# Optimization experiments

Hardware: AMD Instinct MI355X
Metric: run time of the kernel (lower is better)

Reference implementation:

```python
import jax, jax.numpy as jnp
import numpy as np

N, DIN, DOUT = 8192, 256, 128
NEG_SLOPE = 0.01         # F.leaky_relu default
MASK_VAL = -9.0e15       # from the torch source


def setup_inputs() -> dict:
    key = jax.random.key(0)
    kx, kadj, kW, kbW, ka1, ka2, kba = jax.random.split(key, 7)
    x = jax.random.normal(kx, (N, DIN), dtype=jnp.float32)
    adj = jax.random.randint(kadj, (N, N), 0, 2, dtype=jnp.int32)
    # Linear W: input_dim -> output_dim
    W = jax.random.normal(kW, (DIN, DOUT), dtype=jnp.float32) * (1.0 / np.sqrt(DIN))
    bW = jax.random.normal(kbW, (DOUT,), dtype=jnp.float32) * 0.01
    # Linear a: 2*output_dim -> 1, split into the h_i part (a1) and h_j part (a2)
    a1 = jax.random.normal(ka1, (DOUT,), dtype=jnp.float32) * (1.0 / np.sqrt(2 * DOUT))
    a2 = jax.random.normal(ka2, (DOUT,), dtype=jnp.float32) * (1.0 / np.sqrt(2 * DOUT))
    ba = jax.random.normal(kba, (), dtype=jnp.float32) * 0.01
    return {"x": x, "adj": adj, "W": W, "bW": bW, "a1": a1, "a2": a2, "ba": ba}


def reference(x, adj, W, bW, a1, a2, ba):
    # h = W x + b  -> [N, DOUT]
    h = x @ W + bW
    # e[i,j] = leaky_relu(a . [h_i, h_j] + ba) = leaky_relu(a1.h_i + a2.h_j + ba)
    s_src = h @ a1            # [N]
    s_dst = h @ a2            # [N]
    e = s_src[:, None] + s_dst[None, :] + ba   # [N, N]
    e = jnp.where(e > 0, e, NEG_SLOPE * e)
    # mask non-edges, row softmax over neighbors j
    e = jnp.where(adj > 0, e, MASK_VAL)
    alpha = jax.nn.softmax(e, axis=1)          # [N, N]
    # dropout is identity in eval mode (dropout_rate=0)
    return alpha @ h                            # [N, DOUT]
```

## Files before the change

kernel.cpp:

```cpp
#include <hip/hip_runtime.h>
#include <hip/hip_bf16.h>


#define NN 8192
#define DIN 256
#define DOUT 128

typedef __attribute__((ext_vector_type(8))) short short8;
typedef __attribute__((ext_vector_type(4))) float floatx4;

__global__ void prep_wt(const float* __restrict__ W, __hip_bfloat16* __restrict__ WT) {
    int e = blockIdx.x * blockDim.x + threadIdx.x;
    if (e < DIN * DOUT) {
        int k = e >> 7;
        int d = e & 127;
        WT[d * DIN + k] = __float2bfloat16(W[e]);
    }
}

__global__ __launch_bounds__(256, 4) void gat_h(
    const float* __restrict__ x, const __hip_bfloat16* __restrict__ WT,
    const float* __restrict__ bW, const float* __restrict__ a1, const float* __restrict__ a2,
    __hip_bfloat16* __restrict__ hbT, float* __restrict__ s_src, float* __restrict__ s_dst) {
    int tid = threadIdx.x;
    int w = tid >> 6, lane = tid & 63;
    int lm = lane & 15, lq = lane >> 4;
    int i0 = blockIdx.x * 32;
    int r0 = (w >> 1) * 16;
    int c0 = (w & 1) * 64;

    __shared__ float s1s[32], s2s[32];
    if (tid < 32) { s1s[tid] = 0.f; s2s[tid] = 0.f; }
    __syncthreads();

    floatx4 acc[4] = {};
#pragma unroll
    for (int kk = 0; kk < DIN; kk += 32) {
        const float4* xp = (const float4*)&x[(size_t)(i0 + r0 + lm) * DIN + kk + lq * 8];
        float4 xa = xp[0], xb = xp[1];
        union { short8 v; __hip_bfloat16 h[8]; } af;
        af.h[0] = __float2bfloat16(xa.x); af.h[1] = __float2bfloat16(xa.y);
        af.h[2] = __float2bfloat16(xa.z); af.h[3] = __float2bfloat16(xa.w);
        af.h[4] = __float2bfloat16(xb.x); af.h[5] = __float2bfloat16(xb.y);
        af.h[6] = __float2bfloat16(xb.z); af.h[7] = __float2bfloat16(xb.w);
#pragma unroll
        for (int t = 0; t < 4; t++) {
            int d = c0 + 16 * t + lm;
            short8 bf = *(const short8*)&WT[(size_t)d * DIN + kk + lq * 8];
            acc[t] = __builtin_amdgcn_mfma_f32_16x16x32_bf16(af.v, bf, acc[t], 0, 0, 0);
        }
    }
    float s1[4] = {0.f, 0.f, 0.f, 0.f}, s2[4] = {0.f, 0.f, 0.f, 0.f};
#pragma unroll
    for (int t = 0; t < 4; t++) {
        int d = c0 + 16 * t + lm;
        float A1 = a1[d], A2 = a2[d], B = bW[d];
#pragma unroll
        for (int r = 0; r < 4; r++) {
            int row = r0 + lq * 4 + r;
            float h = acc[t][r] + B;
            hbT[(size_t)d * NN + i0 + row] = __float2bfloat16(h);
            s1[r] += h * A1;
            s2[r] += h * A2;
        }
    }
#pragma unroll
    for (int r = 0; r < 4; r++) {
        for (int m = 1; m < 16; m <<= 1) {
            s1[r] += __shfl_xor(s1[r], m, 64);
            s2[r] += __shfl_xor(s2[r], m, 64);
        }
    }
    if (lm == 0) {
#pragma unroll
        for (int r = 0; r < 4; r++) {
            int row = r0 + lq * 4 + r;
            atomicAdd(&s1s[row], s1[r]);
            atomicAdd(&s2s[row], s2[r]);
        }
    }
    __syncthreads();
    if (tid < 32) {
        s_src[i0 + tid] = s1s[tid];
        s_dst[i0 + tid] = s2s[tid];
    }
}

__global__ __launch_bounds__(256, 4) void gat_attn(
    const int* __restrict__ adj, const float* __restrict__ s_src,
    const float* __restrict__ s_dst, const float* __restrict__ ba_p,
    const __hip_bfloat16* __restrict__ hbT,
    float* __restrict__ num, float* __restrict__ lpart, int njt) {
    int tid = threadIdx.x;
    int w = tid >> 6, lane = tid & 63;
    int lm = lane & 15, lq = lane >> 4;
    int b = blockIdx.x;
    int ib = b & 127;
    int jh = b >> 7;
    int i0 = ib * 64 + w * 16;
    int jb0 = jh * (njt * 32);

    float ssi = s_src[i0 + lm] + ba_p[0];

    const int* arow = adj + (size_t)(i0 + lm) * NN + jb0 + lq * 8;
    const float* sd = s_dst + jb0 + lq * 8;
    const __hip_bfloat16* hbb = hbT + (size_t)lm * NN + jb0 + lq * 8;

    floatx4 acc[8] = {};
    floatx4 accd = {};
    const short8 ones = { 0x3F80, 0x3F80, 0x3F80, 0x3F80, 0x3F80, 0x3F80, 0x3F80, 0x3F80 };

    int4 a0 = *(const int4*)arow;
    int4 a1 = *(const int4*)(arow + 4);
    float4 d0 = *(const float4*)sd;
    float4 d1 = *(const float4*)(sd + 4);

    for (int t = 0; t < njt; t++) {
        int4 ca0 = a0, ca1 = a1;
        float4 cd0 = d0, cd1 = d1;
        if (t + 1 < njt) {
            a0 = *(const int4*)(arow + (t + 1) * 32);
            a1 = *(const int4*)(arow + (t + 1) * 32 + 4);
            d0 = *(const float4*)(sd + (t + 1) * 32);
            d1 = *(const float4*)(sd + (t + 1) * 32 + 4);
        }
        float p[8];
        {
            float e;
            e = ssi + cd0.x; e = fmaxf(e, 0.01f * e); p[0] = ca0.x ? __expf(e) : 0.f;
            e = ssi + cd0.y; e = fmaxf(e, 0.01f * e); p[1] = ca0.y ? __expf(e) : 0.f;
            e = ssi + cd0.z; e = fmaxf(e, 0.01f * e); p[2] = ca0.z ? __expf(e) : 0.f;
            e = ssi + cd0.w; e = fmaxf(e, 0.01f * e); p[3] = ca0.w ? __expf(e) : 0.f;
            e = ssi + cd1.x; e = fmaxf(e, 0.01f * e); p[4] = ca1.x ? __expf(e) : 0.f;
            e = ssi + cd1.y; e = fmaxf(e, 0.01f * e); p[5] = ca1.y ? __expf(e) : 0.f;
            e = ssi + cd1.z; e = fmaxf(e, 0.01f * e); p[6] = ca1.z ? __expf(e) : 0.f;
            e = ssi + cd1.w; e = fmaxf(e, 0.01f * e); p[7] = ca1.w ? __expf(e) : 0.f;
        }
        union { short8 v; __hip_bfloat162 q[4]; } af;
        af.q[0] = __float22bfloat162_rn(make_float2(p[0], p[1]));
        af.q[1] = __float22bfloat162_rn(make_float2(p[2], p[3]));
        af.q[2] = __float22bfloat162_rn(make_float2(p[4], p[5]));
        af.q[3] = __float22bfloat162_rn(make_float2(p[6], p[7]));

        size_t off = (size_t)t * 32;
#pragma unroll
        for (int f = 0; f < 8; f++) {
            short8 bf = *(const short8*)(hbb + (size_t)f * 16 * NN + off);
            acc[f] = __builtin_amdgcn_mfma_f32_16x16x32_bf16(af.v, bf, acc[f], 0, 0, 0);
        }
        accd = __builtin_amdgcn_mfma_f32_16x16x32_bf16(af.v, ones, accd, 0, 0, 0);
    }

    float* nb = num + ((size_t)jh * NN + i0) * DOUT;
#pragma unroll
    for (int f = 0; f < 8; f++)
#pragma unroll
        for (int r = 0; r < 4; r++)
            nb[(size_t)(lq * 4 + r) * DOUT + f * 16 + lm] = acc[f][r];
    if (lm == 0) {
#pragma unroll
        for (int r = 0; r < 4; r++)
            lpart[(size_t)jh * NN + i0 + lq * 4 + r] = accd[r];
    }
}

__global__ void gat_combine(const float* __restrict__ num, const float* __restrict__ lpart,
                            float* __restrict__ out, int jsplit) {
    int gid = blockIdx.x * blockDim.x + threadIdx.x;
    int idx = gid * 4;
    int i = idx >> 7;
    float den = 0.f;
    for (int s = 0; s < jsplit; s++) den += lpart[(size_t)s * NN + i];
    float inv = 1.0f / den;
    float4 o = make_float4(0.f, 0.f, 0.f, 0.f);
    for (int s = 0; s < jsplit; s++) {
        float4 n = *(const float4*)&num[(size_t)s * NN * DOUT + idx];
        o.x += n.x; o.y += n.y; o.z += n.z; o.w += n.w;
    }
    o.x *= inv; o.y *= inv; o.z *= inv; o.w *= inv;
    *(float4*)&out[idx] = o;
}

extern "C" void kernel_launch(void* const* d_in, const int* in_sizes, int n_in,
                              void* d_out, int out_size, void* d_ws, size_t ws_size,
                              hipStream_t stream) {
    const float* x  = (const float*)d_in[0];
    const int* adj  = (const int*)d_in[1];
    const float* W  = (const float*)d_in[2];
    const float* bW = (const float*)d_in[3];
    const float* a1 = (const float*)d_in[4];
    const float* a2 = (const float*)d_in[5];
    const float* ba = (const float*)d_in[6];
    float* out = (float*)d_out;

    char* ws = (char*)d_ws;
    __hip_bfloat16* hbT = (__hip_bfloat16*)ws;
    __hip_bfloat16* WT  = (__hip_bfloat16*)(ws + 2097152);
    float* s_src        = (float*)(ws + 2162688);
    float* s_dst        = (float*)(ws + 2195456);
    float* lpart        = (float*)(ws + 2228224);
    float* num          = (float*)(ws + 2490368);

    size_t base = 2490368;
    int jsplit = 2;
    if (ws_size >= base + (size_t)8 * NN * DOUT * 4) jsplit = 8;
    else if (ws_size >= base + (size_t)4 * NN * DOUT * 4) jsplit = 4;
    int njt = NN / (32 * jsplit);

    prep_wt<<<128, 256, 0, stream>>>(W, WT);
    gat_h<<<256, 256, 0, stream>>>(x, WT, bW, a1, a2, hbT, s_src, s_dst);
    gat_attn<<<128 * jsplit, 256, 0, stream>>>(adj, s_src, s_dst, ba, hbT, num, lpart, njt);
    gat_combine<<<1024, 256, 0, stream>>>(num, lpart, out, jsplit);
}
```

Baseline: 512.3 us.

## Pack adjacency into a bitmask in a prepass and template the attention kernel on tile count

Adds a streaming build_mask kernel that compresses each run of eight int32 adjacency entries into a single byte bitmask. The attention kernel then reads one byte per eight columns instead of two int4 loads, which shrinks the per-iteration load footprint and register pressure in the inner MFMA loop. The attention kernel is also templated on the tile count and now prefetches two iterations ahead with partial unrolling. In exchange there is an extra full pass over the 256MB adjacency, an 8MB mask write, and more workspace use; the jsplit=2 fallback is dropped.

```diff
diff --git a/kernel.cpp b/kernel.cpp
--- a/kernel.cpp
+++ b/kernel.cpp
@@ -86,11 +86,28 @@
     }
 }
 
+__global__ void build_mask(const int* __restrict__ adj, unsigned char* __restrict__ mask) {
+    size_t gid = (size_t)blockIdx.x * blockDim.x + threadIdx.x;
+    const int4* a = (const int4*)(adj + gid * 8);
+    int4 v0 = a[0], v1 = a[1];
+    unsigned int b = 0;
+    b |= (v0.x != 0) ? 1u : 0u;
+    b |= (v0.y != 0) ? 2u : 0u;
+    b |= (v0.z != 0) ? 4u : 0u;
+    b |= (v0.w != 0) ? 8u : 0u;
+    b |= (v1.x != 0) ? 16u : 0u;
+    b |= (v1.y != 0) ? 32u : 0u;
+    b |= (v1.z != 0) ? 64u : 0u;
+    b |= (v1.w != 0) ? 128u : 0u;
+    mask[gid] = (unsigned char)b;
+}
+
+template <int NJT>
 __global__ __launch_bounds__(256, 4) void gat_attn(
-    const int* __restrict__ adj, const float* __restrict__ s_src,
+    const unsigned char* __restrict__ mask, const float* __restrict__ s_src,
     const float* __restrict__ s_dst, const float* __restrict__ ba_p,
     const __hip_bfloat16* __restrict__ hbT,
-    float* __restrict__ num, float* __restrict__ lpart, int njt) {
+    float* __restrict__ num, float* __restrict__ lpart) {
     int tid = threadIdx.x;
     int w = tid >> 6, lane = tid & 63;
     int lm = lane & 15, lq = lane >> 4;
@@ -98,11 +115,11 @@
     int ib = b & 127;
     int jh = b >> 7;
     int i0 = ib * 64 + w * 16;
-    int jb0 = jh * (njt * 32);
+    int jb0 = jh * (NJT * 32);
 
     float ssi = s_src[i0 + lm] + ba_p[0];
 
-    const int* arow = adj + (size_t)(i0 + lm) * NN + jb0 + lq * 8;
+    const unsigned char* mrow = mask + (size_t)(i0 + lm) * (NN / 8) + (jb0 >> 3) + lq;
     const float* sd = s_dst + jb0 + lq * 8;
     const __hip_bfloat16* hbb = hbT + (size_t)lm * NN + jb0 + lq * 8;
 
@@ -110,31 +127,34 @@
     floatx4 accd = {};
     const short8 ones = { 0x3F80, 0x3F80, 0x3F80, 0x3F80, 0x3F80, 0x3F80, 0x3F80, 0x3F80 };
 
-    int4 a0 = *(const int4*)arow;
-    int4 a1 = *(const int4*)(arow + 4);
-    float4 d0 = *(const float4*)sd;
-    float4 d1 = *(const float4*)(sd + 4);
-
-    for (int t = 0; t < njt; t++) {
-        int4 ca0 = a0, ca1 = a1;
-        float4 cd0 = d0, cd1 = d1;
-        if (t + 1 < njt) {
-            a0 = *(const int4*)(arow + (t + 1) * 32);
-            a1 = *(const int4*)(arow + (t + 1) * 32 + 4);
-            d0 = *(const float4*)(sd + (t + 1) * 32);
-            d1 = *(const float4*)(sd + (t + 1) * 32 + 4);
+    unsigned int mA = mrow[0];
+    float4 dA0 = *(const float4*)sd;
+    float4 dA1 = *(const float4*)(sd + 4);
+    unsigned int mB = mrow[4];
+    float4 dB0 = *(const float4*)(sd + 32);
+    float4 dB1 = *(const float4*)(sd + 36);
+
+#pragma unroll 4
+    for (int t = 0; t < NJT; t++) {
+        unsigned int cm = mA;
+        float4 cd0 = dA0, cd1 = dA1;
+        mA = mB; dA0 = dB0; dA1 = dB1;
+        if (t + 2 < NJT) {
+            mB = mrow[(t + 2) * 4];
+            dB0 = *(const float4*)(sd + (t + 2) * 32);
+            dB1 = *(const float4*)(sd + (t + 2) * 32 + 4);
         }
         float p[8];
         {
             float e;
-            e = ssi + cd0.x; e = fmaxf(e, 0.01f * e); p[0] = ca0.x ? __expf(e) : 0.f;
-            e = ssi + cd0.y; e = fmaxf(e, 0.01f * e); p[1] = ca0.y ? __expf(e) : 0.f;
-            e = ssi + cd0.z; e = fmaxf(e, 0.01f * e); p[2] = ca0.z ? __expf(e) : 0.f;
-            e = ssi + cd0.w; e = fmaxf(e, 0.01f * e); p[3] = ca0.w ? __expf(e) : 0.f;
-            e = ssi + cd1.x; e = fmaxf(e, 0.01f * e); p[4] = ca1.x ? __expf(e) : 0.f;
-            e = ssi + cd1.y; e = fmaxf(e, 0.01f * e); p[5] = ca1.y ? __expf(e) : 0.f;
-            e = ssi + cd1.z; e = fmaxf(e, 0.01f * e); p[6] = ca1.z ? __expf(e) : 0.f;
-            e = ssi + cd1.w; e = fmaxf(e, 0.01f * e); p[7] = ca1.w ? __expf(e) : 0.f;
+            e = ssi + cd0.x; e = fmaxf(e, 0.01f * e); p[0] = (cm & 1u)   ? __expf(e) : 0.f;
+            e = ssi + cd0.y; e = fmaxf(e, 0.01f * e); p[1] = (cm & 2u)   ? __expf(e) : 0.f;
+            e = ssi + cd0.z; e = fmaxf(e, 0.01f * e); p[2] = (cm & 4u)   ? __expf(e) : 0.f;
+            e = ssi + cd0.w; e = fmaxf(e, 0.01f * e); p[3] = (cm & 8u)   ? __expf(e) : 0.f;
+            e = ssi + cd1.x; e = fmaxf(e, 0.01f * e); p[4] = (cm & 16u)  ? __expf(e) : 0.f;
+            e = ssi + cd1.y; e = fmaxf(e, 0.01f * e); p[5] = (cm & 32u)  ? __expf(e) : 0.f;
+            e = ssi + cd1.z; e = fmaxf(e, 0.01f * e); p[6] = (cm & 64u)  ? __expf(e) : 0.f;
+            e = ssi + cd1.w; e = fmaxf(e, 0.01f * e); p[7] = (cm & 128u) ? __expf(e) : 0.f;
         }
         union { short8 v; __hip_bfloat162 q[4]; } af;
         af.q[0] = __float22bfloat162_rn(make_float2(p[0], p[1]));
@@ -151,7 +171,7 @@
         accd = __builtin_amdgcn_mfma_f32_16x16x32_bf16(af.v, ones, accd, 0, 0, 0);
     }
 
-    float* nb = num + ((size_t)jh * NN + i0) * DOUT;
+    float* nb = num + ((size_t)(b >> 7) * NN + i0) * DOUT;
 #pragma unroll
     for (int f = 0; f < 8; f++)
 #pragma unroll
@@ -160,7 +180,7 @@
     if (lm == 0) {
 #pragma unroll
         for (int r = 0; r < 4; r++)
-            lpart[(size_t)jh * NN + i0 + lq * 4 + r] = accd[r];
+            lpart[(size_t)(b >> 7) * NN + i0 + lq * 4 + r] = accd[r];
     }
 }
 
@@ -194,21 +214,22 @@
     float* out = (float*)d_out;
 
     char* ws = (char*)d_ws;
-    __hip_bfloat16* hbT = (__hip_bfloat16*)ws;
-    __hip_bfloat16* WT  = (__hip_bfloat16*)(ws + 2097152);
-    float* s_src        = (float*)(ws + 2162688);
-    float* s_dst        = (float*)(ws + 2195456);
-    float* lpart        = (float*)(ws + 2228224);
-    float* num          = (float*)(ws + 2490368);
-
-    size_t base = 2490368;
-    int jsplit = 2;
-    if (ws_size >= base + (size_t)8 * NN * DOUT * 4) jsplit = 8;
-    else if (ws_size >= base + (size_t)4 * NN * DOUT * 4) jsplit = 4;
-    int njt = NN / (32 * jsplit);
+    __hip_bfloat16* hbT  = (__hip_bfloat16*)ws;
+    __hip_bfloat16* WT   = (__hip_bfloat16*)(ws + 2097152);
+    float* s_src         = (float*)(ws + 2162688);
+    float* s_dst         = (float*)(ws + 2195456);
+    float* lpart         = (float*)(ws + 2228224);
+    unsigned char* mask  = (unsigned char*)(ws + 2490368);
+    float* num           = (float*)(ws + 10878976);
+
+    int jsplit = (ws_size >= 10878976 + (size_t)8 * NN * DOUT * 4) ? 8 : 4;
 
     prep_wt<<<128, 256, 0, stream>>>(W, WT);
     gat_h<<<256, 256, 0, stream>>>(x, WT, bW, a1, a2, hbT, s_src, s_dst);
-    gat_attn<<<128 * jsplit, 256, 0, stream>>>(adj, s_src, s_dst, ba, hbT, num, lpart, njt);
+    build_mask<<<32768, 256, 0, stream>>>(adj, mask);
+    if (jsplit == 8)
+        gat_attn<32><<<1024, 256, 0, stream>>>(mask, s_src, s_dst, ba, hbT, num, lpart);
+    else
+        gat_attn<64><<<512, 256, 0, stream>>>(mask, s_src, s_dst, ba, hbT, num, lpart);
     gat_combine<<<1024, 256, 0, stream>>>(num, lpart, out, jsplit);
 }
```

Result: slower. 523.5 us (+2.2%).

## Preload adjacency as bitmask, template tile count, use exp2 with prescaled scores

Applied to the files above, without the earlier changes.

The attention kernel now loads its whole adjacency slice up front and packs it into per-lane bitmask registers, so all adj loads are in flight at once instead of one tile ahead. The tile count becomes a template parameter so the loop fully unrolls. Scores are prescaled by log2(e) so the native exp2 instruction replaces __expf. This raises register pressure and front-loads memory traffic, which may reduce occupancy. The jsplit=2 fallback is removed.

```diff
diff --git a/kernel.cpp b/kernel.cpp
--- a/kernel.cpp
+++ b/kernel.cpp
@@ -5,6 +5,7 @@
 #define NN 8192
 #define DIN 256
 #define DOUT 128
+#define LOG2E 1.4426950408889634f
 
 typedef __attribute__((ext_vector_type(8))) short short8;
 typedef __attribute__((ext_vector_type(4))) float floatx4;
@@ -81,16 +82,17 @@
     }
     __syncthreads();
     if (tid < 32) {
-        s_src[i0 + tid] = s1s[tid];
-        s_dst[i0 + tid] = s2s[tid];
-    }
-}
-
+        s_src[i0 + tid] = s1s[tid] * LOG2E;
+        s_dst[i0 + tid] = s2s[tid] * LOG2E;
+    }
+}
+
+template <int NJT>
 __global__ __launch_bounds__(256, 4) void gat_attn(
     const int* __restrict__ adj, const float* __restrict__ s_src,
     const float* __restrict__ s_dst, const float* __restrict__ ba_p,
     const __hip_bfloat16* __restrict__ hbT,
-    float* __restrict__ num, float* __restrict__ lpart, int njt) {
+    float* __restrict__ num, float* __restrict__ lpart) {
     int tid = threadIdx.x;
     int w = tid >> 6, lane = tid & 63;
     int lm = lane & 15, lq = lane >> 4;
@@ -98,11 +100,28 @@
     int ib = b & 127;
     int jh = b >> 7;
     int i0 = ib * 64 + w * 16;
-    int jb0 = jh * (njt * 32);
-
-    float ssi = s_src[i0 + lm] + ba_p[0];
+    int jb0 = jh * (NJT * 32);
 
     const int* arow = adj + (size_t)(i0 + lm) * NN + jb0 + lq * 8;
+    unsigned int mreg[NJT / 4];
+#pragma unroll
+    for (int t = 0; t < NJT; t++) {
+        const int4* ap = (const int4*)(arow + t * 32);
+        int4 v0 = ap[0], v1 = ap[1];
+        unsigned int bb = 0;
+        bb |= (v0.x != 0) ? 1u : 0u;
+        bb |= (v0.y != 0) ? 2u : 0u;
+        bb |= (v0.z != 0) ? 4u : 0u;
+        bb |= (v0.w != 0) ? 8u : 0u;
+        bb |= (v1.x != 0) ? 16u : 0u;
+        bb |= (v1.y != 0) ? 32u : 0u;
+        bb |= (v1.z != 0) ? 64u : 0u;
+        bb |= (v1.w != 0) ? 128u : 0u;
+        if ((t & 3) == 0) mreg[t >> 2] = bb;
+        else              mreg[t >> 2] |= bb << ((t & 3) * 8);
+    }
+
+    float ssi = s_src[i0 + lm] + ba_p[0] * LOG2E;
     const float* sd = s_dst + jb0 + lq * 8;
     const __hip_bfloat16* hbb = hbT + (size_t)lm * NN + jb0 + lq * 8;
 
@@ -110,31 +129,22 @@
     floatx4 accd = {};
     const short8 ones = { 0x3F80, 0x3F80, 0x3F80, 0x3F80, 0x3F80, 0x3F80, 0x3F80, 0x3F80 };
 
-    int4 a0 = *(const int4*)arow;
-    int4 a1 = *(const int4*)(arow + 4);
-    float4 d0 = *(const float4*)sd;
-    float4 d1 = *(const float4*)(sd + 4);
-
-    for (int t = 0; t < njt; t++) {
-        int4 ca0 = a0, ca1 = a1;
-        float4 cd0 = d0, cd1 = d1;
-        if (t + 1 < njt) {
-            a0 = *(const int4*)(arow + (t + 1) * 32);
-            a1 = *(const int4*)(arow + (t + 1) * 32 + 4);
-            d0 = *(const float4*)(sd + (t + 1) * 32);
-            d1 = *(const float4*)(sd + (t + 1) * 32 + 4);
-        }
+#pragma unroll
+    for (int t = 0; t < NJT; t++) {
+        unsigned int cm = (mreg[t >> 2] >> ((t & 3) * 8)) & 0xFFu;
+        float4 cd0 = *(const float4*)(sd + t * 32);
+        float4 cd1 = *(const float4*)(sd + t * 32 + 4);
         float p[8];
         {
             float e;
-            e = ssi + cd0.x; e = fmaxf(e, 0.01f * e); p[0] = ca0.x ? __expf(e) : 0.f;
-            e = ssi + cd0.y; e = fmaxf(e, 0.01f * e); p[1] = ca0.y ? __expf(e) : 0.f;
-            e = ssi + cd0.z; e = fmaxf(e, 0.01f * e); p[2] = ca0.z ? __expf(e) : 0.f;
-            e = ssi + cd0.w; e = fmaxf(e, 0.01f * e); p[3] = ca0.w ? __expf(e) : 0.f;
-            e = ssi + cd1.x; e = fmaxf(e, 0.01f * e); p[4] = ca1.x ? __expf(e) : 0.f;
-            e = ssi + cd1.y; e = fmaxf(e, 0.01f * e); p[5] = ca1.y ? __expf(e) : 0.f;
-            e = ssi + cd1.z; e = fmaxf(e, 0.01f * e); p[6] = ca1.z ? __expf(e) : 0.f;
-            e = ssi + cd1.w; e = fmaxf(e, 0.01f * e); p[7] = ca1.w ? __expf(e) : 0.f;
+            e = ssi + cd0.x; e = fmaxf(e, 0.01f * e); p[0] = (cm & 1u)   ? __builtin_amdgcn_exp2f(e) : 0.f;
+            e = ssi + cd0.y; e = fmaxf(e, 0.01f * e); p[1] = (cm & 2u)   ? __builtin_amdgcn_exp2f(e) : 0.f;
+            e = ssi + cd0.z; e = fmaxf(e, 0.01f * e); p[2] = (cm & 4u)   ? __builtin_amdgcn_exp2f(e) : 0.f;
+            e = ssi + cd0.w; e = fmaxf(e, 0.01f * e); p[3] = (cm & 8u)   ? __builtin_amdgcn_exp2f(e) : 0.f;
+            e = ssi + cd1.x; e = fmaxf(e, 0.01f * e); p[4] = (cm & 16u)  ? __builtin_amdgcn_exp2f(e) : 0.f;
+            e = ssi + cd1.y; e = fmaxf(e, 0.01f * e); p[5] = (cm & 32u)  ? __builtin_amdgcn_exp2f(e) : 0.f;
+            e = ssi + cd1.z; e = fmaxf(e, 0.01f * e); p[6] = (cm & 64u)  ? __builtin_amdgcn_exp2f(e) : 0.f;
+            e = ssi + cd1.w; e = fmaxf(e, 0.01f * e); p[7] = (cm & 128u) ? __builtin_amdgcn_exp2f(e) : 0.f;
         }
         union { short8 v; __hip_bfloat162 q[4]; } af;
         af.q[0] = __float22bfloat162_rn(make_float2(p[0], p[1]));
@@ -194,21 +204,20 @@
     float* out = (float*)d_out;
 
     char* ws = (char*)d_ws;
-    __hip_bfloat16* hbT = (__hip_bfloat16*)ws;
-    __hip_bfloat16* WT  = (__hip_bfloat16*)(ws + 2097152);
-    float* s_src        = (float*)(ws + 2162688);
-    float* s_dst        = (float*)(ws + 2195456);
-    float* lpart        = (float*)(ws + 2228224);
-    float* num          = (float*)(ws + 2490368);
-
-    size_t base = 2490368;
-    int jsplit = 2;
-    if (ws_size >= base + (size_t)8 * NN * DOUT * 4) jsplit = 8;
-    else if (ws_size >= base + (size_t)4 * NN * DOUT * 4) jsplit = 4;
-    int njt = NN / (32 * jsplit);
+    __hip_bfloat16* hbT  = (__hip_bfloat16*)ws;
+    __hip_bfloat16* WT   = (__hip_bfloat16*)(ws + 2097152);
+    float* s_src         = (float*)(ws + 2162688);
+    float* s_dst         = (float*)(ws + 2195456);
+    float* lpart         = (float*)(ws + 2228224);
+    float* num           = (float*)(ws + 2490368);
+
+    int jsplit = (ws_size >= 2490368 + (size_t)8 * NN * DOUT * 4) ? 8 : 4;
 
     prep_wt<<<128, 256, 0, stream>>>(W, WT);
     gat_h<<<256, 256, 0, stream>>>(x, WT, bW, a1, a2, hbT, s_src, s_dst);
-    gat_attn<<<128 * jsplit, 256, 0, stream>>>(adj, s_src, s_dst, ba, hbT, num, lpart, njt);
+    if (jsplit == 8)
+        gat_attn<32><<<1024, 256, 0, stream>>>(adj, s_src, s_dst, ba, hbT, num, lpart);
+    else
+        gat_attn<64><<<512, 256, 0, stream>>>(adj, s_src, s_dst, ba, hbT, num, lpart);
     gat_combine<<<1024, 256, 0, stream>>>(num, lpart, out, jsplit);
 }
```

Result: no change. 504.1 us (-1.6%).
